# Kernel tuning notes

Hardware: AMD Instinct MI355X
Metric: run time of the kernel (lower is better)

Reference implementation:

```python
import jax, jax.numpy as jnp
import numpy as np
from jax import lax

CONTEXT_DIM = 256
HIDDEN_DIM = 128
OUTPUT_DIM = 2
INPUT_DIM = OUTPUT_DIM + CONTEXT_DIM  # 258
BATCH = 16384
PRED_LEN = 48
DT = 1.0 / 30.0


def setup_inputs() -> dict:
    key = jax.random.key(0)
    ks = jax.random.split(key, 12)
    s = 0.05
    return {
        "context": jax.random.normal(ks[0], (BATCH, CONTEXT_DIM), jnp.float32),
        "last_velocity": jax.random.normal(ks[1], (BATCH, OUTPUT_DIM), jnp.float32),
        # init_hidden: Linear(context_dim -> hidden_dim * num_layers) + Tanh
        "W_init": jax.random.normal(ks[2], (HIDDEN_DIM, CONTEXT_DIM), jnp.float32) * s,
        "b_init": jax.random.normal(ks[3], (HIDDEN_DIM,), jnp.float32) * s,
        # GRU (single layer), PyTorch layout: [3*hidden, in] with gate order r,z,n
        "W_ih": jax.random.normal(ks[4], (3 * HIDDEN_DIM, INPUT_DIM), jnp.float32) * s,
        "b_ih": jax.random.normal(ks[5], (3 * HIDDEN_DIM,), jnp.float32) * s,
        "W_hh": jax.random.normal(ks[6], (3 * HIDDEN_DIM, HIDDEN_DIM), jnp.float32) * s,
        "b_hh": jax.random.normal(ks[7], (3 * HIDDEN_DIM,), jnp.float32) * s,
        # delta_output MLP: Linear(128->64), ReLU, Linear(64->2)
        "W1": jax.random.normal(ks[8], (HIDDEN_DIM // 2, HIDDEN_DIM), jnp.float32) * s,
        "b1": jax.random.normal(ks[9], (HIDDEN_DIM // 2,), jnp.float32) * s,
        "W2": jax.random.normal(ks[10], (OUTPUT_DIM, HIDDEN_DIM // 2), jnp.float32) * s,
        "b2": jax.random.normal(ks[11], (OUTPUT_DIM,), jnp.float32) * s,
        "pred_len": PRED_LEN,
    }


def reference(context, last_velocity, W_init, b_init, W_ih, b_ih, W_hh, b_hh,
              W1, b1, W2, b2, pred_len):
    # initial hidden state: tanh(Linear(context))  -> [B, H]
    h0 = jnp.tanh(context @ W_init.T + b_init)
    delta0 = last_velocity * DT            # current_delta = last_velocity * dt
    pos0 = jnp.zeros_like(delta0)          # current_pos = 0

    def step(carry, _):
        delta, h, pos = carry
        x = jnp.concatenate([delta, context], axis=1)        # [B, 258]
        gi = x @ W_ih.T + b_ih                               # [B, 3H]
        gh = h @ W_hh.T + b_hh                               # [B, 3H]
        i_r, i_z, i_n = jnp.split(gi, 3, axis=1)
        h_r, h_z, h_n = jnp.split(gh, 3, axis=1)
        r = jax.nn.sigmoid(i_r + h_r)
        z = jax.nn.sigmoid(i_z + h_z)
        n = jnp.tanh(i_n + r * h_n)
        h_new = (1.0 - z) * n + z * h                        # GRU update
        hid = jax.nn.relu(h_new @ W1.T + b1)                 # [B, 64]
        pred_delta = hid @ W2.T + b2                         # [B, 2]
        pos_new = pos + pred_delta
        return (pred_delta, h_new, pos_new), pos_new

    _, positions = lax.scan(step, (delta0, h0, pos0), None, length=int(pred_len))
    return jnp.transpose(positions, (1, 0, 2))               # [B, T, 2]
```

## Files before the change

### kernel.cpp

```cpp
#include <hip/hip_runtime.h>
#include <stdint.h>

#define TPB 512
#define BM 32
#define CTXD 256
#define HID 128
#define TSTEPS 48
#define DTC (1.0f/30.0f)

typedef short short8 __attribute__((ext_vector_type(8)));
typedef float f32x4 __attribute__((ext_vector_type(4)));
typedef float f32x2 __attribute__((ext_vector_type(2)));

#define OFF_WN   0
#define OFF_W1   32768
#define OFF_H    49152
#define HBUFSZ   8192
#define CSTRIDE  512
#define OFF_PART 65536
#define OFF_TWDR 66560
#define OFF_TWDZ 67072
#define OFF_TWDN 67584
#define OFF_TBHN 68096
#define OFF_TB1  68608
#define OFF_TW2  68864
#define OFF_GIN  69632
#define LDS_BYTES 77824

__device__ __forceinline__ uint32_t cvtpk_bf16(float lo, float hi) {
    uint32_t r;
    asm("v_cvt_pk_bf16_f32 %0, %1, %2" : "=v"(r) : "v"(lo), "v"(hi));
    return r;
}
__device__ __forceinline__ uint32_t pkh2(float a, float b) {
    union { _Float16 h[2]; uint32_t u; } v;
    v.h[0] = (_Float16)a; v.h[1] = (_Float16)b; return v.u;
}
__device__ __forceinline__ float h2lo(uint32_t u) {
    union { uint32_t u; _Float16 h[2]; } v; v.u = u; return (float)v.h[0];
}
__device__ __forceinline__ float h2hi(uint32_t u) {
    union { uint32_t u; _Float16 h[2]; } v; v.u = u; return (float)v.h[1];
}
__device__ __forceinline__ float fsigm(float x) {
    return __builtin_amdgcn_rcpf(1.0f + __expf(-x));
}
__device__ __forceinline__ float ftanhf(float x) {
    return fmaf(-2.0f, __builtin_amdgcn_rcpf(1.0f + __expf(2.0f * x)), 1.0f);
}
__device__ __forceinline__ short8 ldA8(const float* src) {
    f32x2 v0 = *(const f32x2*)(src + 0);
    f32x2 v1 = *(const f32x2*)(src + 2);
    f32x2 v2 = *(const f32x2*)(src + 4);
    f32x2 v3 = *(const f32x2*)(src + 6);
    union { short8 s; uint32_t u[4]; } r;
    r.u[0] = cvtpk_bf16(v0.x, v0.y);
    r.u[1] = cvtpk_bf16(v1.x, v1.y);
    r.u[2] = cvtpk_bf16(v2.x, v2.y);
    r.u[3] = cvtpk_bf16(v3.x, v3.y);
    return r.s;
}

__global__ __launch_bounds__(TPB, 3)
void dd_kernel(const float* __restrict__ ctx, const float* __restrict__ lv,
               const float* __restrict__ Winit, const float* __restrict__ binit,
               const float* __restrict__ Wih, const float* __restrict__ bih,
               const float* __restrict__ Whh, const float* __restrict__ bhh,
               const float* __restrict__ W1, const float* __restrict__ b1,
               const float* __restrict__ W2, const float* __restrict__ b2,
               float* __restrict__ out)
{
    extern __shared__ char smem[];
    const int tid  = threadIdx.x;
    const int w    = tid >> 6;
    const int lane = tid & 63;
    const int g    = (lane >> 4) & 3;
    const int l15  = lane & 15;
    const int row0 = blockIdx.x * BM;
    const int jt   = w & 3;
    const int msel = (w >> 2) & 1;

    for (int p = tid; p < 128 * 64; p += TPB) {
        int u = p >> 6, kp = p & 63;
        f32x2 v = *(const f32x2*)(Whh + (size_t)(256 + u) * HID + 2 * kp);
        *(uint32_t*)(smem + OFF_WN + u * 256 + ((4 * kp) ^ ((u & 15) << 4))) = cvtpk_bf16(v.x, v.y);
    }
    for (int p = tid; p < 64 * 64; p += TPB) {
        int u = p >> 6, kp = p & 63;
        f32x2 v = *(const f32x2*)(W1 + u * HID + 2 * kp);
        *(uint32_t*)(smem + OFF_W1 + u * 256 + ((4 * kp) ^ ((u & 15) << 4))) = cvtpk_bf16(v.x, v.y);
    }
    for (int p = tid; p < 32 * 128; p += TPB) {
        int r = p >> 7, kp = p & 127;
        f32x2 v = *(const f32x2*)(ctx + (size_t)(row0 + r) * CTXD + 2 * kp);
        *(uint32_t*)(smem + OFF_H + r * CSTRIDE + ((4 * kp) ^ ((r & 15) << 4))) = cvtpk_bf16(v.x, v.y);
    }
    if (tid < 128) {
        int u = tid;
        *(uint32_t*)(smem + OFF_TWDR + u * 4) = pkh2(Wih[(size_t)u * 258], Wih[(size_t)u * 258 + 1]);
        *(uint32_t*)(smem + OFF_TWDZ + u * 4) = pkh2(Wih[(size_t)(128 + u) * 258], Wih[(size_t)(128 + u) * 258 + 1]);
        *(uint32_t*)(smem + OFF_TWDN + u * 4) = pkh2(Wih[(size_t)(256 + u) * 258], Wih[(size_t)(256 + u) * 258 + 1]);
        *(float*)(smem + OFF_TBHN + u * 4) = bhh[256 + u];
        *(float*)(smem + OFF_TW2 + u * 4) = W2[u];
    }
    if (tid < 64) *(float*)(smem + OFF_TB1 + tid * 4) = b1[tid];

    const int u16 = 16 * w + l15;
    const float b2c0 = b2[0], b2c1 = b2[1];
    float dx[2], dy[2], pos0[2], pos1[2];
#pragma unroll
    for (int m = 0; m < 2; ++m) {
        f32x2 v = *(const f32x2*)(lv + (size_t)(row0 + 16 * m + l15) * 2);
        dx[m] = v.x * DTC; dy[m] = v.y * DTC;
        pos0[m] = 0.f; pos1[m] = 0.f;
    }

    __syncthreads();

    f32x4 zero4 = {0.f, 0.f, 0.f, 0.f};
    f32x4 accA[4][2];
#pragma unroll
    for (int jl = 0; jl < 4; ++jl) { accA[jl][0] = zero4; accA[jl][1] = zero4; }

    const int cswz = (16 * g) ^ (l15 << 4);
    for (int kk = 0; kk < 8; ++kk) {
        const int cx = cswz ^ (64 * kk);
        short8 bf0 = *(const short8*)(smem + OFF_H + l15 * CSTRIDE + cx);
        short8 bf1 = *(const short8*)(smem + OFF_H + (16 + l15) * CSTRIDE + cx);
        short8 afR = ldA8(Wih + (size_t)u16 * 258 + 2 + 32 * kk + 8 * g);
        short8 afZ = ldA8(Wih + (size_t)(128 + u16) * 258 + 2 + 32 * kk + 8 * g);
        short8 afN = ldA8(Wih + (size_t)(256 + u16) * 258 + 2 + 32 * kk + 8 * g);
        short8 afH = ldA8(Winit + (size_t)u16 * 256 + 32 * kk + 8 * g);
        accA[0][0] = __builtin_amdgcn_mfma_f32_16x16x32_bf16(afR, bf0, accA[0][0], 0, 0, 0);
        accA[0][1] = __builtin_amdgcn_mfma_f32_16x16x32_bf16(afR, bf1, accA[0][1], 0, 0, 0);
        accA[1][0] = __builtin_amdgcn_mfma_f32_16x16x32_bf16(afZ, bf0, accA[1][0], 0, 0, 0);
        accA[1][1] = __builtin_amdgcn_mfma_f32_16x16x32_bf16(afZ, bf1, accA[1][1], 0, 0, 0);
        accA[2][0] = __builtin_amdgcn_mfma_f32_16x16x32_bf16(afN, bf0, accA[2][0], 0, 0, 0);
        accA[2][1] = __builtin_amdgcn_mfma_f32_16x16x32_bf16(afN, bf1, accA[2][1], 0, 0, 0);
        accA[3][0] = __builtin_amdgcn_mfma_f32_16x16x32_bf16(afH, bf0, accA[3][0], 0, 0, 0);
        accA[3][1] = __builtin_amdgcn_mfma_f32_16x16x32_bf16(afH, bf1, accA[3][1], 0, 0, 0);
    }

    uint32_t gipR[2][2], gipZ[2][2];
    float hm[2][4];
    {
        const int ub = 16 * w + 4 * g;
        float tbr[4], tbz[4], tbn[4], thi[4];
#pragma unroll
        for (int r = 0; r < 4; ++r) {
            int u = ub + r;
            tbr[r] = bih[u] + bhh[u];
            tbz[r] = bih[128 + u] + bhh[128 + u];
            tbn[r] = bih[256 + u];
            thi[r] = binit[u];
        }
        uint4 gn4;
        gn4.x = pkh2(accA[2][0][0] + tbn[0], accA[2][0][1] + tbn[1]);
        gn4.y = pkh2(accA[2][0][2] + tbn[2], accA[2][0][3] + tbn[3]);
        gn4.z = pkh2(accA[2][1][0] + tbn[0], accA[2][1][1] + tbn[1]);
        gn4.w = pkh2(accA[2][1][2] + tbn[2], accA[2][1][3] + tbn[3]);
        *(uint4*)(smem + OFF_GIN + tid * 16) = gn4;
#pragma unroll
        for (int m = 0; m < 2; ++m) {
            gipR[m][0] = pkh2(accA[0][m][0] + tbr[0], accA[0][m][1] + tbr[1]);
            gipR[m][1] = pkh2(accA[0][m][2] + tbr[2], accA[0][m][3] + tbr[3]);
            gipZ[m][0] = pkh2(accA[1][m][0] + tbz[0], accA[1][m][1] + tbz[1]);
            gipZ[m][1] = pkh2(accA[1][m][2] + tbz[2], accA[1][m][3] + tbz[3]);
#pragma unroll
            for (int r = 0; r < 4; ++r)
                hm[m][r] = ftanhf(accA[3][m][r] + thi[r]);
        }
    }

    short8 wfr[4], wfz[4];
#pragma unroll
    for (int kk = 0; kk < 4; ++kk) {
        wfr[kk] = ldA8(Whh + (size_t)u16 * HID + 32 * kk + 8 * g);
        wfz[kk] = ldA8(Whh + (size_t)(128 + u16) * HID + 32 * kk + 8 * g);
    }

    __syncthreads();

    const int hwcol = (32 * w + 8 * g) ^ (l15 << 4);
#pragma unroll
    for (int m = 0; m < 2; ++m) {
        uint2 pk;
        pk.x = cvtpk_bf16(hm[m][0], hm[m][1]);
        pk.y = cvtpk_bf16(hm[m][2], hm[m][3]);
        *(uint2*)(smem + OFF_H + (16 * m + l15) * 256 + hwcol) = pk;
    }
    __syncthreads();

    const int uNb = OFF_WN + u16 * 256;
    const int uWb = OFF_W1 + (16 * jt + l15) * 256;
    const int hrow0 = l15 * 256;
    const int hrow1 = (16 + l15) * 256;
    const int ub4 = (16 * w + 4 * g) * 4;
    const int um4 = (16 * jt + 4 * g) * 4;

    for (int t = 0; t <= TSTEPS; ++t) {
        const int rbuf = OFF_H + (t & 1) * HBUFSZ;
        const int wbuf = OFF_H + ((t + 1) & 1) * HBUFSZ;
        f32x4 aR[2], aZ[2], aN[2];
        f32x4 a1 = zero4;
        if (t < TSTEPS) {
            f32x4 bh = *(const f32x4*)(smem + OFF_TBHN + ub4);
#pragma unroll
            for (int m = 0; m < 2; ++m) {
                aR[m][0] = h2lo(gipR[m][0]); aR[m][1] = h2hi(gipR[m][0]);
                aR[m][2] = h2lo(gipR[m][1]); aR[m][3] = h2hi(gipR[m][1]);
                aZ[m][0] = h2lo(gipZ[m][0]); aZ[m][1] = h2hi(gipZ[m][0]);
                aZ[m][2] = h2lo(gipZ[m][1]); aZ[m][3] = h2hi(gipZ[m][1]);
                aN[m] = bh;
            }
#pragma unroll
            for (int kk = 0; kk < 4; ++kk) {
                const int cx = cswz ^ (64 * kk);
                short8 bf0 = *(const short8*)(smem + rbuf + hrow0 + cx);
                short8 bf1 = *(const short8*)(smem + rbuf + hrow1 + cx);
                short8 fN  = *(const short8*)(smem + uNb + cx);
                short8 wfk = *(const short8*)(smem + uWb + cx);
                aR[0] = __builtin_amdgcn_mfma_f32_16x16x32_bf16(wfr[kk], bf0, aR[0], 0, 0, 0);
                aR[1] = __builtin_amdgcn_mfma_f32_16x16x32_bf16(wfr[kk], bf1, aR[1], 0, 0, 0);
                aZ[0] = __builtin_amdgcn_mfma_f32_16x16x32_bf16(wfz[kk], bf0, aZ[0], 0, 0, 0);
                aZ[1] = __builtin_amdgcn_mfma_f32_16x16x32_bf16(wfz[kk], bf1, aZ[1], 0, 0, 0);
                aN[0] = __builtin_amdgcn_mfma_f32_16x16x32_bf16(fN, bf0, aN[0], 0, 0, 0);
                aN[1] = __builtin_amdgcn_mfma_f32_16x16x32_bf16(fN, bf1, aN[1], 0, 0, 0);
                short8 bfM = msel ? bf1 : bf0;
                a1 = __builtin_amdgcn_mfma_f32_16x16x32_bf16(wfk, bfM, a1, 0, 0, 0);
            }
        } else {
#pragma unroll
            for (int kk = 0; kk < 4; ++kk) {
                const int cx = cswz ^ (64 * kk);
                short8 bfM = *(const short8*)(smem + rbuf + (msel ? hrow1 : hrow0) + cx);
                short8 wfk = *(const short8*)(smem + uWb + cx);
                a1 = __builtin_amdgcn_mfma_f32_16x16x32_bf16(wfk, bfM, a1, 0, 0, 0);
            }
        }
        {
            f32x4 b1v = *(const f32x4*)(smem + OFF_TB1 + um4);
            f32x4 w2a = *(const f32x4*)(smem + OFF_TW2 + um4);
            f32x4 w2b = *(const f32x4*)(smem + OFF_TW2 + 256 + um4);
            float s0 = 0.f, s1 = 0.f;
#pragma unroll
            for (int r = 0; r < 4; ++r) {
                float hv = fmaxf(a1[r] + b1v[r], 0.f);
                s0 = fmaf(hv, w2a[r], s0);
                s1 = fmaf(hv, w2b[r], s1);
            }
            s0 += __shfl_xor(s0, 16, 64); s0 += __shfl_xor(s0, 32, 64);
            s1 += __shfl_xor(s1, 16, 64); s1 += __shfl_xor(s1, 32, 64);
            if (lane < 16) {
                f32x2 pw; pw.x = s0; pw.y = s1;
                *(f32x2*)(smem + OFF_PART + msel * 512 + l15 * 32 + jt * 8) = pw;
            }
        }
        __syncthreads();
        if (t > 0) {
#pragma unroll
            for (int m = 0; m < 2; ++m) {
                f32x4 q0 = *(const f32x4*)(smem + OFF_PART + m * 512 + l15 * 32);
                f32x4 q1 = *(const f32x4*)(smem + OFF_PART + m * 512 + l15 * 32 + 16);
                float pdx = (q0[0] + q0[2]) + (q1[0] + q1[2]) + b2c0;
                float pdy = (q0[1] + q0[3]) + (q1[1] + q1[3]) + b2c1;
                dx[m] = pdx; dy[m] = pdy;
                pos0[m] += pdx; pos1[m] += pdy;
            }
            if (w == 0 && lane < 16) {
#pragma unroll
                for (int m = 0; m < 2; ++m) {
                    f32x2 o2; o2.x = pos0[m]; o2.y = pos1[m];
                    *(f32x2*)(out + (size_t)(row0 + 16 * m + l15) * (TSTEPS * 2) + 2 * (t - 1)) = o2;
                }
            }
        }
        if (t < TSTEPS) {
            uint4 twr = *(const uint4*)(smem + OFF_TWDR + ub4);
            uint4 twz = *(const uint4*)(smem + OFF_TWDZ + ub4);
            uint4 twn = *(const uint4*)(smem + OFF_TWDN + ub4);
            uint4 gn4 = *(const uint4*)(smem + OFF_GIN + tid * 16);
            uint32_t twru[4] = {twr.x, twr.y, twr.z, twr.w};
            uint32_t twzu[4] = {twz.x, twz.y, twz.z, twz.w};
            uint32_t twnu[4] = {twn.x, twn.y, twn.z, twn.w};
            uint32_t gnu[4]  = {gn4.x, gn4.y, gn4.z, gn4.w};
#pragma unroll
            for (int m = 0; m < 2; ++m) {
#pragma unroll
                for (int r = 0; r < 4; ++r) {
                    float rr  = fsigm(fmaf(dy[m], h2hi(twru[r]), fmaf(dx[m], h2lo(twru[r]), aR[m][r])));
                    float zz  = fsigm(fmaf(dy[m], h2hi(twzu[r]), fmaf(dx[m], h2lo(twzu[r]), aZ[m][r])));
                    float gnv = (r & 1) ? h2hi(gnu[2 * m + (r >> 1)]) : h2lo(gnu[2 * m + (r >> 1)]);
                    float inn = fmaf(dy[m], h2hi(twnu[r]), fmaf(dx[m], h2lo(twnu[r]), gnv));
                    float nn  = ftanhf(fmaf(rr, aN[m][r], inn));
                    hm[m][r]  = fmaf(zz, hm[m][r] - nn, nn);
                }
                uint2 pk;
                pk.x = cvtpk_bf16(hm[m][0], hm[m][1]);
                pk.y = cvtpk_bf16(hm[m][2], hm[m][3]);
                *(uint2*)(smem + wbuf + (16 * m + l15) * 256 + hwcol) = pk;
            }
        }
        __syncthreads();
    }
}

extern "C" void kernel_launch(void* const* d_in, const int* in_sizes, int n_in,
                              void* d_out, int out_size, void* d_ws, size_t ws_size,
                              hipStream_t stream) {
    (void)in_sizes; (void)n_in; (void)d_ws; (void)ws_size; (void)out_size;
    const float* ctx   = (const float*)d_in[0];
    const float* lv    = (const float*)d_in[1];
    const float* Winit = (const float*)d_in[2];
    const float* binit = (const float*)d_in[3];
    const float* Wih   = (const float*)d_in[4];
    const float* bih   = (const float*)d_in[5];
    const float* Whh   = (const float*)d_in[6];
    const float* bhh   = (const float*)d_in[7];
    const float* W1    = (const float*)d_in[8];
    const float* b1    = (const float*)d_in[9];
    const float* W2    = (const float*)d_in[10];
    const float* b2    = (const float*)d_in[11];
    float* out = (float*)d_out;

    hipFuncSetAttribute(reinterpret_cast<const void*>(dd_kernel),
                        hipFuncAttributeMaxDynamicSharedMemorySize, LDS_BYTES);
    dd_kernel<<<16384 / BM, TPB, LDS_BYTES, stream>>>(
        ctx, lv, Winit, binit, Wih, bih, Whh, bhh, W1, b1, W2, b2, out);
}
```

Baseline: 204.0 us.

## Compute output MLP redundantly per wave to drop a barrier per timestep

```diff
diff --git a/kernel.cpp b/kernel.cpp
--- a/kernel.cpp
+++ b/kernel.cpp
@@ -12,20 +12,17 @@
 typedef float f32x4 __attribute__((ext_vector_type(4)));
 typedef float f32x2 __attribute__((ext_vector_type(2)));
 
-#define OFF_WN   0
-#define OFF_W1   32768
-#define OFF_H    49152
+#define OFF_WZ   0
+#define OFF_WN   32768
+#define OFF_H    65536
 #define HBUFSZ   8192
 #define CSTRIDE  512
-#define OFF_PART 65536
-#define OFF_TWDR 66560
-#define OFF_TWDZ 67072
-#define OFF_TWDN 67584
-#define OFF_TBHN 68096
-#define OFF_TB1  68608
-#define OFF_TW2  68864
-#define OFF_GIN  69632
-#define LDS_BYTES 77824
+#define OFF_GIN  81920
+#define OFF_WD   90112
+#define OFF_BHN  93184
+#define OFF_TB1  93696
+#define OFF_TW2  93952
+#define LDS_BYTES 94464
 
 __device__ __forceinline__ uint32_t cvtpk_bf16(float lo, float hi) {
     uint32_t r;
@@ -61,7 +58,7 @@
     return r.s;
 }
 
-__global__ __launch_bounds__(TPB, 3)
+__global__ __launch_bounds__(TPB, 2)
 void dd_kernel(const float* __restrict__ ctx, const float* __restrict__ lv,
                const float* __restrict__ Winit, const float* __restrict__ binit,
                const float* __restrict__ Wih, const float* __restrict__ bih,
@@ -77,19 +74,18 @@
     const int g    = (lane >> 4) & 3;
     const int l15  = lane & 15;
     const int row0 = blockIdx.x * BM;
-    const int jt   = w & 3;
-    const int msel = (w >> 2) & 1;
-
+    const int swz  = l15 << 4;
+
+    for (int p = tid; p < 128 * 64; p += TPB) {
+        int u = p >> 6, kp = p & 63;
+        f32x2 v = *(const f32x2*)(Whh + (size_t)(128 + u) * HID + 2 * kp);
+        *(uint32_t*)(smem + OFF_WZ + u * 256 + ((4 * kp) ^ ((u & 15) << 4))) = cvtpk_bf16(v.x, v.y);
+    }
     for (int p = tid; p < 128 * 64; p += TPB) {
         int u = p >> 6, kp = p & 63;
         f32x2 v = *(const f32x2*)(Whh + (size_t)(256 + u) * HID + 2 * kp);
         *(uint32_t*)(smem + OFF_WN + u * 256 + ((4 * kp) ^ ((u & 15) << 4))) = cvtpk_bf16(v.x, v.y);
     }
-    for (int p = tid; p < 64 * 64; p += TPB) {
-        int u = p >> 6, kp = p & 63;
-        f32x2 v = *(const f32x2*)(W1 + u * HID + 2 * kp);
-        *(uint32_t*)(smem + OFF_W1 + u * 256 + ((4 * kp) ^ ((u & 15) << 4))) = cvtpk_bf16(v.x, v.y);
-    }
     for (int p = tid; p < 32 * 128; p += TPB) {
         int r = p >> 7, kp = p & 127;
         f32x2 v = *(const f32x2*)(ctx + (size_t)(row0 + r) * CTXD + 2 * kp);
@@ -97,13 +93,16 @@
     }
     if (tid < 128) {
         int u = tid;
-        *(uint32_t*)(smem + OFF_TWDR + u * 4) = pkh2(Wih[(size_t)u * 258], Wih[(size_t)u * 258 + 1]);
-        *(uint32_t*)(smem + OFF_TWDZ + u * 4) = pkh2(Wih[(size_t)(128 + u) * 258], Wih[(size_t)(128 + u) * 258 + 1]);
-        *(uint32_t*)(smem + OFF_TWDN + u * 4) = pkh2(Wih[(size_t)(256 + u) * 258], Wih[(size_t)(256 + u) * 258 + 1]);
-        *(float*)(smem + OFF_TBHN + u * 4) = bhh[256 + u];
-        *(float*)(smem + OFF_TW2 + u * 4) = W2[u];
-    }
-    if (tid < 64) *(float*)(smem + OFF_TB1 + tid * 4) = b1[tid];
+        ((float*)(smem + OFF_WD +    0))[u] = Wih[(size_t)u * 258 + 0];
+        ((float*)(smem + OFF_WD +  512))[u] = Wih[(size_t)u * 258 + 1];
+        ((float*)(smem + OFF_WD + 1024))[u] = Wih[(size_t)(128 + u) * 258 + 0];
+        ((float*)(smem + OFF_WD + 1536))[u] = Wih[(size_t)(128 + u) * 258 + 1];
+        ((float*)(smem + OFF_WD + 2048))[u] = Wih[(size_t)(256 + u) * 258 + 0];
+        ((float*)(smem + OFF_WD + 2560))[u] = Wih[(size_t)(256 + u) * 258 + 1];
+        ((float*)(smem + OFF_BHN))[u] = bhh[256 + u];
+        ((float*)(smem + OFF_TW2))[u] = W2[u];
+    }
+    if (tid < 64) ((float*)(smem + OFF_TB1))[tid] = b1[tid];
 
     const int u16 = 16 * w + l15;
     const float b2c0 = b2[0], b2c1 = b2[1];
@@ -122,11 +121,10 @@
 #pragma unroll
     for (int jl = 0; jl < 4; ++jl) { accA[jl][0] = zero4; accA[jl][1] = zero4; }
 
-    const int cswz = (16 * g) ^ (l15 << 4);
     for (int kk = 0; kk < 8; ++kk) {
-        const int cx = cswz ^ (64 * kk);
-        short8 bf0 = *(const short8*)(smem + OFF_H + l15 * CSTRIDE + cx);
-        short8 bf1 = *(const short8*)(smem + OFF_H + (16 + l15) * CSTRIDE + cx);
+        const int cx = (64 * kk + 16 * g);
+        short8 bf0 = *(const short8*)(smem + OFF_H + l15 * CSTRIDE + (cx ^ swz));
+        short8 bf1 = *(const short8*)(smem + OFF_H + (16 + l15) * CSTRIDE + (cx ^ swz));
         short8 afR = ldA8(Wih + (size_t)u16 * 258 + 2 + 32 * kk + 8 * g);
         short8 afZ = ldA8(Wih + (size_t)(128 + u16) * 258 + 2 + 32 * kk + 8 * g);
         short8 afN = ldA8(Wih + (size_t)(256 + u16) * 258 + 2 + 32 * kk + 8 * g);
@@ -144,11 +142,10 @@
     uint32_t gipR[2][2], gipZ[2][2];
     float hm[2][4];
     {
-        const int ub = 16 * w + 4 * g;
         float tbr[4], tbz[4], tbn[4], thi[4];
 #pragma unroll
         for (int r = 0; r < 4; ++r) {
-            int u = ub + r;
+            int u = 16 * w + 4 * g + r;
             tbr[r] = bih[u] + bhh[u];
             tbz[r] = bih[128 + u] + bhh[128 + u];
             tbn[r] = bih[256 + u];
@@ -172,39 +169,40 @@
         }
     }
 
-    short8 wfr[4], wfz[4];
+    short8 wfr[4], wf1[4][4];
 #pragma unroll
     for (int kk = 0; kk < 4; ++kk) {
         wfr[kk] = ldA8(Whh + (size_t)u16 * HID + 32 * kk + 8 * g);
-        wfz[kk] = ldA8(Whh + (size_t)(128 + u16) * HID + 32 * kk + 8 * g);
+#pragma unroll
+        for (int jt = 0; jt < 4; ++jt)
+            wf1[jt][kk] = ldA8(W1 + (size_t)(16 * jt + l15) * HID + 32 * kk + 8 * g);
     }
 
     __syncthreads();
 
-    const int hwcol = (32 * w + 8 * g) ^ (l15 << 4);
 #pragma unroll
     for (int m = 0; m < 2; ++m) {
         uint2 pk;
         pk.x = cvtpk_bf16(hm[m][0], hm[m][1]);
         pk.y = cvtpk_bf16(hm[m][2], hm[m][3]);
-        *(uint2*)(smem + OFF_H + (16 * m + l15) * 256 + hwcol) = pk;
+        *(uint2*)(smem + OFF_H + (16 * m + l15) * 256 + ((32 * w + 8 * g) ^ swz)) = pk;
     }
     __syncthreads();
 
-    const int uNb = OFF_WN + u16 * 256;
-    const int uWb = OFF_W1 + (16 * jt + l15) * 256;
-    const int hrow0 = l15 * 256;
-    const int hrow1 = (16 + l15) * 256;
+    short8 hf[2][4];
+#pragma unroll
+    for (int m = 0; m < 2; ++m)
+#pragma unroll
+        for (int kk = 0; kk < 4; ++kk)
+            hf[m][kk] = *(const short8*)(smem + OFF_H + (16 * m + l15) * 256 + ((64 * kk + 16 * g) ^ swz));
+
     const int ub4 = (16 * w + 4 * g) * 4;
-    const int um4 = (16 * jt + 4 * g) * 4;
-
-    for (int t = 0; t <= TSTEPS; ++t) {
-        const int rbuf = OFF_H + (t & 1) * HBUFSZ;
+
+    for (int t = 0; t < TSTEPS; ++t) {
         const int wbuf = OFF_H + ((t + 1) & 1) * HBUFSZ;
         f32x4 aR[2], aZ[2], aN[2];
-        f32x4 a1 = zero4;
-        if (t < TSTEPS) {
-            f32x4 bh = *(const f32x4*)(smem + OFF_TBHN + ub4);
+        {
+            f32x4 bh = *(const f32x4*)(smem + OFF_BHN + ub4);
 #pragma unroll
             for (int m = 0; m < 2; ++m) {
                 aR[m][0] = h2lo(gipR[m][0]); aR[m][1] = h2hi(gipR[m][0]);
@@ -213,95 +211,90 @@
                 aZ[m][2] = h2lo(gipZ[m][1]); aZ[m][3] = h2hi(gipZ[m][1]);
                 aN[m] = bh;
             }
-#pragma unroll
-            for (int kk = 0; kk < 4; ++kk) {
-                const int cx = cswz ^ (64 * kk);
-                short8 bf0 = *(const short8*)(smem + rbuf + hrow0 + cx);
-                short8 bf1 = *(const short8*)(smem + rbuf + hrow1 + cx);
-                short8 fN  = *(const short8*)(smem + uNb + cx);
-                short8 wfk = *(const short8*)(smem + uWb + cx);
-                aR[0] = __builtin_amdgcn_mfma_f32_16x16x32_bf16(wfr[kk], bf0, aR[0], 0, 0, 0);
-                aR[1] = __builtin_amdgcn_mfma_f32_16x16x32_bf16(wfr[kk], bf1, aR[1], 0, 0, 0);
-                aZ[0] = __builtin_amdgcn_mfma_f32_16x16x32_bf16(wfz[kk], bf0, aZ[0], 0, 0, 0);
-                aZ[1] = __builtin_amdgcn_mfma_f32_16x16x32_bf16(wfz[kk], bf1, aZ[1], 0, 0, 0);
-                aN[0] = __builtin_amdgcn_mfma_f32_16x16x32_bf16(fN, bf0, aN[0], 0, 0, 0);
-                aN[1] = __builtin_amdgcn_mfma_f32_16x16x32_bf16(fN, bf1, aN[1], 0, 0, 0);
-                short8 bfM = msel ? bf1 : bf0;
-                a1 = __builtin_amdgcn_mfma_f32_16x16x32_bf16(wfk, bfM, a1, 0, 0, 0);
-            }
-        } else {
-#pragma unroll
-            for (int kk = 0; kk < 4; ++kk) {
-                const int cx = cswz ^ (64 * kk);
-                short8 bfM = *(const short8*)(smem + rbuf + (msel ? hrow1 : hrow0) + cx);
-                short8 wfk = *(const short8*)(smem + uWb + cx);
-                a1 = __builtin_amdgcn_mfma_f32_16x16x32_bf16(wfk, bfM, a1, 0, 0, 0);
+        }
+#pragma unroll
+        for (int kk = 0; kk < 4; ++kk) {
+            const int cx = (64 * kk + 16 * g) ^ swz;
+            short8 fZ = *(const short8*)(smem + OFF_WZ + u16 * 256 + cx);
+            short8 fN = *(const short8*)(smem + OFF_WN + u16 * 256 + cx);
+#pragma unroll
+            for (int m = 0; m < 2; ++m) {
+                aR[m] = __builtin_amdgcn_mfma_f32_16x16x32_bf16(wfr[kk], hf[m][kk], aR[m], 0, 0, 0);
+                aZ[m] = __builtin_amdgcn_mfma_f32_16x16x32_bf16(fZ, hf[m][kk], aZ[m], 0, 0, 0);
+                aN[m] = __builtin_amdgcn_mfma_f32_16x16x32_bf16(fN, hf[m][kk], aN[m], 0, 0, 0);
             }
         }
         {
-            f32x4 b1v = *(const f32x4*)(smem + OFF_TB1 + um4);
-            f32x4 w2a = *(const f32x4*)(smem + OFF_TW2 + um4);
-            f32x4 w2b = *(const f32x4*)(smem + OFF_TW2 + 256 + um4);
-            float s0 = 0.f, s1 = 0.f;
-#pragma unroll
-            for (int r = 0; r < 4; ++r) {
-                float hv = fmaxf(a1[r] + b1v[r], 0.f);
-                s0 = fmaf(hv, w2a[r], s0);
-                s1 = fmaf(hv, w2b[r], s1);
-            }
-            s0 += __shfl_xor(s0, 16, 64); s0 += __shfl_xor(s0, 32, 64);
-            s1 += __shfl_xor(s1, 16, 64); s1 += __shfl_xor(s1, 32, 64);
-            if (lane < 16) {
-                f32x2 pw; pw.x = s0; pw.y = s1;
-                *(f32x2*)(smem + OFF_PART + msel * 512 + l15 * 32 + jt * 8) = pw;
-            }
-        }
-        __syncthreads();
-        if (t > 0) {
+            f32x4 wr0 = *(const f32x4*)(smem + OFF_WD +    0 + ub4);
+            f32x4 wr1 = *(const f32x4*)(smem + OFF_WD +  512 + ub4);
+            f32x4 wz0 = *(const f32x4*)(smem + OFF_WD + 1024 + ub4);
+            f32x4 wz1 = *(const f32x4*)(smem + OFF_WD + 1536 + ub4);
+            f32x4 wn0 = *(const f32x4*)(smem + OFF_WD + 2048 + ub4);
+            f32x4 wn1 = *(const f32x4*)(smem + OFF_WD + 2560 + ub4);
+            uint4 gn4 = *(const uint4*)(smem + OFF_GIN + tid * 16);
+            uint32_t gnu[4] = {gn4.x, gn4.y, gn4.z, gn4.w};
 #pragma unroll
             for (int m = 0; m < 2; ++m) {
-                f32x4 q0 = *(const f32x4*)(smem + OFF_PART + m * 512 + l15 * 32);
-                f32x4 q1 = *(const f32x4*)(smem + OFF_PART + m * 512 + l15 * 32 + 16);
-                float pdx = (q0[0] + q0[2]) + (q1[0] + q1[2]) + b2c0;
-                float pdy = (q0[1] + q0[3]) + (q1[1] + q1[3]) + b2c1;
-                dx[m] = pdx; dy[m] = pdy;
-                pos0[m] += pdx; pos1[m] += pdy;
-            }
-            if (w == 0 && lane < 16) {
-#pragma unroll
-                for (int m = 0; m < 2; ++m) {
-                    f32x2 o2; o2.x = pos0[m]; o2.y = pos1[m];
-                    *(f32x2*)(out + (size_t)(row0 + 16 * m + l15) * (TSTEPS * 2) + 2 * (t - 1)) = o2;
-                }
-            }
-        }
-        if (t < TSTEPS) {
-            uint4 twr = *(const uint4*)(smem + OFF_TWDR + ub4);
-            uint4 twz = *(const uint4*)(smem + OFF_TWDZ + ub4);
-            uint4 twn = *(const uint4*)(smem + OFF_TWDN + ub4);
-            uint4 gn4 = *(const uint4*)(smem + OFF_GIN + tid * 16);
-            uint32_t twru[4] = {twr.x, twr.y, twr.z, twr.w};
-            uint32_t twzu[4] = {twz.x, twz.y, twz.z, twz.w};
-            uint32_t twnu[4] = {twn.x, twn.y, twn.z, twn.w};
-            uint32_t gnu[4]  = {gn4.x, gn4.y, gn4.z, gn4.w};
-#pragma unroll
-            for (int m = 0; m < 2; ++m) {
 #pragma unroll
                 for (int r = 0; r < 4; ++r) {
-                    float rr  = fsigm(fmaf(dy[m], h2hi(twru[r]), fmaf(dx[m], h2lo(twru[r]), aR[m][r])));
-                    float zz  = fsigm(fmaf(dy[m], h2hi(twzu[r]), fmaf(dx[m], h2lo(twzu[r]), aZ[m][r])));
+                    float rr  = fsigm(fmaf(dy[m], wr1[r], fmaf(dx[m], wr0[r], aR[m][r])));
+                    float zz  = fsigm(fmaf(dy[m], wz1[r], fmaf(dx[m], wz0[r], aZ[m][r])));
                     float gnv = (r & 1) ? h2hi(gnu[2 * m + (r >> 1)]) : h2lo(gnu[2 * m + (r >> 1)]);
-                    float inn = fmaf(dy[m], h2hi(twnu[r]), fmaf(dx[m], h2lo(twnu[r]), gnv));
+                    float inn = fmaf(dy[m], wn1[r], fmaf(dx[m], wn0[r], gnv));
                     float nn  = ftanhf(fmaf(rr, aN[m][r], inn));
                     hm[m][r]  = fmaf(zz, hm[m][r] - nn, nn);
                 }
                 uint2 pk;
                 pk.x = cvtpk_bf16(hm[m][0], hm[m][1]);
                 pk.y = cvtpk_bf16(hm[m][2], hm[m][3]);
-                *(uint2*)(smem + wbuf + (16 * m + l15) * 256 + hwcol) = pk;
+                *(uint2*)(smem + wbuf + (16 * m + l15) * 256 + ((32 * w + 8 * g) ^ swz)) = pk;
             }
         }
         __syncthreads();
+#pragma unroll
+        for (int m = 0; m < 2; ++m)
+#pragma unroll
+            for (int kk = 0; kk < 4; ++kk)
+                hf[m][kk] = *(const short8*)(smem + wbuf + (16 * m + l15) * 256 + ((64 * kk + 16 * g) ^ swz));
+        float s0[2] = {0.f, 0.f}, s1[2] = {0.f, 0.f};
+#pragma unroll
+        for (int jt = 0; jt < 4; ++jt) {
+            f32x4 a10 = zero4, a11 = zero4;
+#pragma unroll
+            for (int kk = 0; kk < 4; ++kk) {
+                a10 = __builtin_amdgcn_mfma_f32_16x16x32_bf16(wf1[jt][kk], hf[0][kk], a10, 0, 0, 0);
+                a11 = __builtin_amdgcn_mfma_f32_16x16x32_bf16(wf1[jt][kk], hf[1][kk], a11, 0, 0, 0);
+            }
+            const int um4 = (16 * jt + 4 * g) * 4;
+            f32x4 b1v = *(const f32x4*)(smem + OFF_TB1 + um4);
+            f32x4 w2a = *(const f32x4*)(smem + OFF_TW2 + um4);
+            f32x4 w2b = *(const f32x4*)(smem + OFF_TW2 + 256 + um4);
+#pragma unroll
+            for (int r = 0; r < 4; ++r) {
+                float h0v = fmaxf(a10[r] + b1v[r], 0.f);
+                float h1v = fmaxf(a11[r] + b1v[r], 0.f);
+                s0[0] = fmaf(h0v, w2a[r], s0[0]);
+                s1[0] = fmaf(h0v, w2b[r], s1[0]);
+                s0[1] = fmaf(h1v, w2a[r], s0[1]);
+                s1[1] = fmaf(h1v, w2b[r], s1[1]);
+            }
+        }
+#pragma unroll
+        for (int m = 0; m < 2; ++m) {
+            float a = s0[m], b = s1[m];
+            a += __shfl_xor(a, 16, 64); a += __shfl_xor(a, 32, 64);
+            b += __shfl_xor(b, 16, 64); b += __shfl_xor(b, 32, 64);
+            a += b2c0; b += b2c1;
+            dx[m] = a; dy[m] = b;
+            pos0[m] += a; pos1[m] += b;
+        }
+        if (w == 0 && lane < 16) {
+#pragma unroll
+            for (int m = 0; m < 2; ++m) {
+                f32x2 o2; o2.x = pos0[m]; o2.y = pos1[m];
+                *(f32x2*)(out + (size_t)(row0 + 16 * m + l15) * (TSTEPS * 2) + 2 * t) = o2;
+            }
+        }
     }
 }
 
```

Result: slower. 276.7 us (+35.6%).
